# Optimization experiments

Hardware: AMD Instinct MI355X
Metric: run time of the kernel (lower is better)

## Reference

```python
import jax, jax.numpy as jnp
import numpy as np
from functools import partial

B, L, V = 64, 512, 20000
P, M = 150, 6          # total patterns, max pattern length
NEG = -1e9             # semiring zero (log-space)
END_STATES = np.repeat(np.array([3, 4, 5]), 50)  # pattern_len-1 per pattern


@jax.custom_vjp
def ste_heaviside(x):
    return (x > 0).astype(x.dtype)

def _ste_fwd(x):
    return ste_heaviside(x), None

def _ste_bwd(_, g):
    return (g,)  # straight-through identity (matches torch code path)

ste_heaviside.defvjp(_ste_fwd, _ste_bwd)


def setup_inputs() -> dict:
    key = jax.random.key(0)
    ks = jax.random.split(key, 8)
    return {
        "docs": jax.random.randint(ks[0], (B, L), 0, V),
        "doc_lens": jax.random.randint(ks[1], (B,), 1, L),
        "local_embeddings": jax.random.normal(ks[2], (300, V), jnp.float32),
        "diags": jax.random.normal(ks[3], (P * M, 300), jnp.float32) * 0.05,
        "bias": jax.random.normal(ks[4], (P * M, 1), jnp.float32) * 0.05,
        "wildcards": jax.random.normal(ks[5], (P, M - 1), jnp.float32) * 0.05,
        "ln_gamma": jnp.ones((P,), jnp.float32),
        "ln_beta": jnp.zeros((P,), jnp.float32),
        "linear_w": jax.random.normal(ks[6], (2, P), jnp.float32) * 0.05,
        "linear_b": jnp.zeros((2,), jnp.float32),
    }


def reference(docs, doc_lens, local_embeddings, diags, bias, wildcards,
              ln_gamma, ln_beta, linear_w, linear_b):
    end_states = jnp.asarray(END_STATES)                  # [P]
    pat_idx = jnp.arange(P)

    # transition matrices over local vocab, mapped into log-space semiring
    tm_vocab = jax.nn.log_sigmoid((diags @ local_embeddings + bias).T)  # [V, P*M]
    tm = tm_vocab[docs].reshape(B, L, P, M)               # [B,L,P,M]

    # wildcard transitions: semiring.times(one=0, log_sigmoid(wildcards))
    wild = jax.nn.log_sigmoid(wildcards)                  # [P, M-1]

    restart = jnp.zeros((B, P, 1), tm.dtype)              # semiring one
    hid0 = jnp.full((B, P, M), NEG, tm.dtype).at[:, :, 0].set(0.0)
    scores0 = jnp.full((B, P), NEG, tm.dtype)             # semiring zero

    def step(carry, inputs):
        hid, sc = carry
        t, tm_t = inputs                                  # tm_t: [B,P,M]
        main = jnp.concatenate([restart, hid[:, :, :-1] + tm_t[:, :, :-1]], axis=2)
        wildp = jnp.concatenate([restart, hid[:, :, :-1] + wild[None]], axis=2)
        hid = jnp.maximum(main, wildp)                    # semiring plus
        esv = hid[:, pat_idx, end_states]                 # [B,P]
        active = (doc_lens > t)[:, None]
        sc = jnp.where(active, jnp.maximum(sc, esv), sc)
        return (hid, sc), None

    xs = (jnp.arange(L), jnp.moveaxis(tm, 1, 0))          # [L], [L,B,P,M]
    (_, scores), _ = jax.lax.scan(step, (hid0, scores0), xs)

    scores = jnp.exp(scores)                              # from_semiring_to_outer
    mu = scores.mean(axis=-1, keepdims=True)
    var = scores.var(axis=-1, keepdims=True)
    norm = (scores - mu) * jax.lax.rsqrt(var + 1e-5) * ln_gamma + ln_beta
    binar = ste_heaviside(norm)
    return binar @ linear_w.T + linear_b
```

## Files before the change

### kernel.cpp

```cpp
#include <hip/hip_runtime.h>
#include <hip/hip_bf16.h>
#include <hip/hip_fp16.h>
#include <math.h>

#define B_   64
#define L_   512
#define V_   20000
#define P_   150
#define M_   6
#define KDIM 300
#define NOUT 750
#define CWS  752
#define NEGF (-1.0e9f)

#define BM 128
#define BN 128
#define BK 16
#define LDP 132

#define KP 320
#define NIT 10
#define NVG 157
#define NJ  6
#define TILE_U4 1024
#define SA 1024.0f
#define SB 16384.0f
#define INV24 (5.9604644775390625e-8f)

#define TCHUNK 32
#define NCHUNK (L_ / TCHUNK)
#define WARM   5
#define CS_STRIDE 160
#define KVBUF 3

typedef _Float16 f16x8 __attribute__((ext_vector_type(8)));
typedef float f32x16 __attribute__((ext_vector_type(16)));

__device__ __forceinline__ float logsigf(float x) {
    return fminf(x, 0.f) - log1pf(expf(-fabsf(x)));
}

__device__ __forceinline__ float logsigf_fast(float x) {
    return fminf(x, 0.f) - __logf(1.f + __expf(-fabsf(x)));
}

__device__ __forceinline__ void gload_lds16(const void* gp, void* lp) {
    __builtin_amdgcn_global_load_lds(
        (const __attribute__((address_space(1))) unsigned int*)gp,
        (__attribute__((address_space(3))) unsigned int*)lp, 16, 0, 0);
}


__global__ __launch_bounds__(256) void p12_split(
    const float* __restrict__ emb, const float* __restrict__ diags,
    uint4* __restrict__ a_t, uint4* __restrict__ b_t)
{
    __shared__ float T[64][132];
    const int t   = threadIdx.x;
    const int bid = blockIdx.x;

    if (bid < NVG * 5) {
        const int gx = bid % NVG;
        const int ky = bid / NVG;
        const int v0 = gx * 128;
        const int k0 = ky * 64;

        #pragma unroll
        for (int pass = 0; pass < 8; ++pass) {
            int flat = pass * 256 + t;
            int krow = flat >> 5;
            int c4   = (flat & 31) * 4;
            int kg   = k0 + krow;
            int v    = v0 + c4;
            float4 f = {0.f, 0.f, 0.f, 0.f};
            if (kg < KDIM && v + 3 < V_)
                f = *(const float4*)(emb + (size_t)kg * V_ + v);
            *(float4*)&T[krow][c4] = f;
        }
        __syncthreads();

        const int vv = t >> 1;
        const int kh = (t & 1) * 32;
        const int it = ky * 2 + (kh >> 5);
        const int v  = v0 + vv;
        if (v < V_) {
            union { ushort u[8]; uint4 q; } H[4], Lo[4];
            #pragma unroll
            for (int i = 0; i < 32; ++i) {
                float x = T[kh + i][vv] * SA;
                __half h = __float2half_rn(x);
                float rem = x - __half2float(h);
                H[i >> 3].u[i & 7]  = __half_as_ushort(h);
                Lo[i >> 3].u[i & 7] = __half_as_ushort(__float2half_rn(rem));
            }
            uint4* tile = a_t + ((size_t)gx * NIT + it) * TILE_U4;
            #pragma unroll
            for (int c = 0; c < 4; ++c) {
                tile[      c * 128 + vv] = H[c].q;
                tile[512 + c * 128 + vv] = Lo[c].q;
            }
        }
    } else {
        const int bidx = bid - NVG * 5;
        const int it   = bidx % NIT;
        const int j    = bidx / NIT;
        const int row  = t >> 1;
        const int qh   = (t & 1) * 2;
        const int n    = j * 128 + row;
        const bool nok = (n < NOUT);
        const int pm   = nok ? ((n / 5) * 6 + (n % 5)) : 0;
        uint4* tile = b_t + (size_t)bidx * TILE_U4;
        #pragma unroll
        for (int qq = 0; qq < 2; ++qq) {
            int q = qh + qq;
            union { ushort u[8]; uint4 v; } H, Lo;
            #pragma unroll
            for (int e = 0; e < 8; ++e) {
                int k = it * 32 + q * 8 + e;
                float x = (nok && k < KDIM) ? diags[(size_t)pm * KDIM + k] * SB : 0.f;
                __half h = __float2half_rn(x);
                float rem = x - __half2float(h);
                H.u[e]  = __half_as_ushort(h);
                Lo.u[e] = __half_as_ushort(__float2half_rn(rem));
            }
            tile[      q * 128 + row] = H.v;
            tile[512 + q * 128 + row] = Lo.v;
        }
    }
}

__global__ __attribute__((amdgpu_waves_per_eu(2, 2))) __launch_bounds__(256)
void k1m_gemm(
    const uint4* __restrict__ a_t, const uint4* __restrict__ b_t,
    const float* __restrict__ bias, const float* __restrict__ wildc,
    float* __restrict__ cw)
{
    const int bid  = blockIdx.x;
    const int xcd  = bid & 7;
    const int slot = bid >> 3;
    const int g    = xcd + 8 * (slot / 6);
    const int j    = slot % 6;
    if (g >= NVG) return;

    const int t    = threadIdx.x;
    const int lane = t & 63;
    const int w    = t >> 6;
    const int wr   = w >> 1, wc = w & 1;
    const int v0   = g * 128;
    const int n0   = j * 128;

    const int fk16 = lane >> 5;
    const int fm   = lane & 31;

    const uint4* abase = a_t + (size_t)g * NIT * TILE_U4;
    const uint4* bbase = b_t + (size_t)j * NIT * TILE_U4;

    f32x16 acc[2][2];
    #pragma unroll
    for (int i = 0; i < 2; ++i)
        #pragma unroll
        for (int jj = 0; jj < 2; ++jj)
            #pragma unroll
            for (int e = 0; e < 16; ++e) acc[i][jj][e] = 0.f;

    #pragma unroll
    for (int it = 0; it < NIT; ++it) {
        const uint4* atile = abase + (size_t)it * TILE_U4;
        const uint4* btile = bbase + (size_t)it * TILE_U4;
        #pragma unroll
        for (int s = 0; s < 2; ++s) {
            const int q = s * 2 + fk16;
            f16x8 A1[2], A2[2], B1[2], B2[2];
            #pragma unroll
            for (int ri = 0; ri < 2; ++ri) {
                const uint4* ap = atile + q * 128 + wr * 64 + ri * 32 + fm;
                A1[ri] = *(const f16x8*)ap;
                A2[ri] = *(const f16x8*)(ap + 512);
            }
            #pragma unroll
            for (int cj = 0; cj < 2; ++cj) {
                const uint4* bp = btile + q * 128 + wc * 64 + cj * 32 + fm;
                B1[cj] = *(const f16x8*)bp;
                B2[cj] = *(const f16x8*)(bp + 512);
            }
            #pragma unroll
            for (int ri = 0; ri < 2; ++ri)
                #pragma unroll
                for (int cj = 0; cj < 2; ++cj) {
                    acc[ri][cj] = __builtin_amdgcn_mfma_f32_32x32x16_f16(A1[ri], B1[cj], acc[ri][cj], 0, 0, 0);
                    acc[ri][cj] = __builtin_amdgcn_mfma_f32_32x32x16_f16(A1[ri], B2[cj], acc[ri][cj], 0, 0, 0);
                    acc[ri][cj] = __builtin_amdgcn_mfma_f32_32x32x16_f16(A2[ri], B1[cj], acc[ri][cj], 0, 0, 0);
                }
        }
    }

    float biasv[2], lwv[2]; int ncol[2]; bool nok[2];
    #pragma unroll
    for (int cj = 0; cj < 2; ++cj) {
        int n = n0 + wc * 64 + cj * 32 + fm;
        ncol[cj] = n;
        nok[cj]  = (n < NOUT);
        int nc = nok[cj] ? n : 0;
        int pm = (nc / 5) * 6 + (nc % 5);
        biasv[cj] = bias[pm];
        lwv[cj]   = logsigf_fast(wildc[nc]);
    }
    #pragma unroll
    for (int ri = 0; ri < 2; ++ri) {
        int vbase = v0 + wr * 64 + ri * 32 + 4 * fk16;
        #pragma unroll
        for (int cj = 0; cj < 2; ++cj) {
            if (!nok[cj]) continue;
            #pragma unroll
            for (int e = 0; e < 16; ++e) {
                int v = vbase + (e & 3) + 8 * (e >> 2);
                if (v < V_) {
                    float val = acc[ri][cj][e] * INV24 + biasv[cj];
                    cw[(size_t)v * CWS + ncol[cj]] = fmaxf(logsigf_fast(val), lwv[cj]);
                }
            }
        }
    }
}


__global__ __launch_bounds__(256) void k1_gemm_cw(
    const float* __restrict__ emb,
    const float* __restrict__ diags,
    const float* __restrict__ bias,
    const float* __restrict__ wildc,
    float* __restrict__ cw)
{
    __shared__ float As[BK][LDP];
    __shared__ float Bs[BK][LDP];

    const int tid = threadIdx.x;
    const int v0 = blockIdx.x * BM;
    const int n0 = blockIdx.y * BN;
    const int tx = tid & 15;
    const int ty = tid >> 4;

    float acc[8][8];
    #pragma unroll
    for (int i = 0; i < 8; ++i)
        #pragma unroll
        for (int j = 0; j < 8; ++j) acc[i][j] = 0.f;

    const int a_k = tid >> 4;
    const int a_v = (tid & 15) * 8;
    const int b_n   = tid >> 1;
    const int b_kof = (tid & 1) * 8;

    int  brow;
    bool bval;
    {
        int n = n0 + b_n;
        bval = (n < NOUT);
        brow = bval ? ((n / 5) * 6 + (n % 5)) : 0;
    }

    for (int k0 = 0; k0 < KDIM; k0 += BK) {
        {
            float4 f0 = {0,0,0,0}, f1 = {0,0,0,0};
            int k = k0 + a_k;
            if (k < KDIM) {
                const float* src = emb + (size_t)k * V_ + v0 + a_v;
                if (v0 + a_v + 3 < V_) f0 = *(const float4*)src;
                if (v0 + a_v + 7 < V_) f1 = *(const float4*)(src + 4);
            }
            *(float4*)&As[a_k][a_v]     = f0;
            *(float4*)&As[a_k][a_v + 4] = f1;
        }
        {
            float4 f = {0,0,0,0}, g = {0,0,0,0};
            if (bval) {
                const float* src = diags + (size_t)brow * KDIM + k0 + b_kof;
                if (k0 + b_kof + 3 < KDIM) f = *(const float4*)src;
                if (k0 + b_kof + 7 < KDIM) g = *(const float4*)(src + 4);
            }
            Bs[b_kof + 0][b_n] = f.x;
            Bs[b_kof + 1][b_n] = f.y;
            Bs[b_kof + 2][b_n] = f.z;
            Bs[b_kof + 3][b_n] = f.w;
            Bs[b_kof + 4][b_n] = g.x;
            Bs[b_kof + 5][b_n] = g.y;
            Bs[b_kof + 6][b_n] = g.z;
            Bs[b_kof + 7][b_n] = g.w;
        }
        __syncthreads();
        #pragma unroll
        for (int k = 0; k < BK; ++k) {
            float4 a0 = *(const float4*)&As[k][tx * 4];
            float4 a1 = *(const float4*)&As[k][64 + tx * 4];
            float4 b0 = *(const float4*)&Bs[k][ty * 8];
            float4 b1 = *(const float4*)&Bs[k][ty * 8 + 4];
            float av[8] = {a0.x, a0.y, a0.z, a0.w, a1.x, a1.y, a1.z, a1.w};
            float bv[8] = {b0.x, b0.y, b0.z, b0.w, b1.x, b1.y, b1.z, b1.w};
            #pragma unroll
            for (int i = 0; i < 8; ++i)
                #pragma unroll
                for (int j = 0; j < 8; ++j)
                    acc[i][j] = fmaf(av[i], bv[j], acc[i][j]);
        }
        __syncthreads();
    }

    float biasv[8], lwv[8];
    #pragma unroll
    for (int j = 0; j < 8; ++j) {
        int n  = n0 + ty * 8 + j;
        int nc = (n < NOUT) ? n : 0;
        int pm = (nc / 5) * 6 + (nc % 5);
        biasv[j] = bias[pm];
        lwv[j]   = logsigf(wildc[nc]);
    }
    #pragma unroll
    for (int i = 0; i < 8; ++i) {
        int v = v0 + ((i < 4) ? (tx * 4 + i) : (64 + tx * 4 + (i - 4)));
        if (v >= V_) continue;
        float r[8];
        #pragma unroll
        for (int j = 0; j < 8; ++j)
            r[j] = fmaxf(logsigf(acc[i][j] + biasv[j]), lwv[j]);
        float* dst = cw + (size_t)v * CWS + n0 + ty * 8;
        if (n0 + ty * 8     < NOUT) *(float4*)dst       = make_float4(r[0], r[1], r[2], r[3]);
        if (n0 + ty * 8 + 4 < NOUT) *(float4*)(dst + 4) = make_float4(r[4], r[5], r[6], r[7]);
    }
}


__global__ __launch_bounds__(192) void k2_scan(
    const int* __restrict__ docs,
    const int* __restrict__ doc_lens,
    const float* __restrict__ cw,
    float* __restrict__ cs)
{
    const int ci = blockIdx.x;
    const int b  = blockIdx.y;
    const int t0 = ci * TCHUNK;
    const int ts = (t0 >= WARM) ? (t0 - WARM) : 0;
    const int dl = doc_lens[b];
    const int te = min(t0 + TCHUNK, dl);
    const int nt = te - ts;

    __shared__ int   toks[TCHUNK + WARM];
    __shared__ float rows[KVBUF][3][768];

    const int t    = threadIdx.x;
    const int lane = t & 63;
    const int w    = t >> 6;

    if (t < TCHUNK + WARM) {
        int tt = ts + t;
        toks[t] = docs[b * L_ + min(tt, L_ - 1)];
    }
    __syncthreads();

    const int p      = t;
    const int e      = (p < 50) ? 3 : (p < 100) ? 4 : 5;
    const int warm_n = t0 - ts;
    float h1 = NEGF, h2 = NEGF, h3 = NEGF, h4 = NEGF, h5 = NEGF, sc = NEGF;

    const int nrounds = (nt > 0) ? (nt + 2) / 3 : 0;

    for (int r0 = 0; r0 < 2; ++r0) {
        if (r0 >= nrounds) break;
        int idx = min(3 * r0 + w, nt - 1);
        const char* rowp = (const char*)(cw + (size_t)toks[idx] * CWS);
        char* lbase = (char*)&rows[r0][w][0];
        #pragma unroll
        for (int jj = 0; jj < 3; ++jj)
            gload_lds16(rowp + jj * 1024 + lane * 16,
                        lbase + jj * 1024 + lane * 16);
    }

    int bufc = 0;
    for (int r = 0; r < nrounds; ++r) {
        if (r + 1 < nrounds) {
            asm volatile("s_waitcnt vmcnt(3)" ::: "memory");
        } else {
            asm volatile("s_waitcnt vmcnt(0)" ::: "memory");
        }
        __builtin_amdgcn_s_barrier();
        asm volatile("" ::: "memory");

        if (r + 2 < nrounds) {
            int rn  = r + 2;
            int idx = min(3 * rn + w, nt - 1);
            const char* rowp = (const char*)(cw + (size_t)toks[idx] * CWS);
            int bn = bufc + 2; if (bn >= KVBUF) bn -= KVBUF;
            char* lbase = (char*)&rows[bn][w][0];
            #pragma unroll
            for (int jj = 0; jj < 3; ++jj)
                gload_lds16(rowp + jj * 1024 + lane * 16,
                            lbase + jj * 1024 + lane * 16);
        }

        #pragma unroll
        for (int u = 0; u < 3; ++u) {
            int i2 = 3 * r + u;
            if (i2 >= nt) break;
            if (p < P_) {
                const float* rp = &rows[bufc][u][p * 5];
                float c0 = rp[0], c1 = rp[1], c2 = rp[2], c3 = rp[3], c4 = rp[4];
                h5 = h4 + c4;
                h4 = h3 + c3;
                h3 = h2 + c2;
                h2 = h1 + c1;
                h1 = c0;
                if (i2 >= warm_n) {
                    float esv = (e == 3) ? h3 : (e == 4) ? h4 : h5;
                    sc = fmaxf(sc, esv);
                }
            }
        }
        bufc = (bufc + 1 == KVBUF) ? 0 : bufc + 1;
    }
    if (p < P_) cs[(size_t)(b * NCHUNK + ci) * CS_STRIDE + p] = sc;
}

__device__ __forceinline__ float block_sum192(float v, volatile float* red, int tid) {
    #pragma unroll
    for (int off = 32; off > 0; off >>= 1) v += __shfl_down(v, off, 64);
    __syncthreads();
    if ((tid & 63) == 0) red[tid >> 6] = v;
    __syncthreads();
    return red[0] + red[1] + red[2];
}

__global__ __launch_bounds__(192) void k3_final(
    const float* __restrict__ cs,
    const float* __restrict__ gamma,
    const float* __restrict__ beta,
    const float* __restrict__ lw,
    const float* __restrict__ lb,
    float* __restrict__ out)
{
    __shared__ float red[3];
    const int b   = blockIdx.x;
    const int tid = threadIdx.x;
    float s = 0.f;
    if (tid < P_) {
        float m = NEGF;
        const float* row = cs + (size_t)b * NCHUNK * CS_STRIDE + tid;
        #pragma unroll
        for (int ci = 0; ci < NCHUNK; ++ci) m = fmaxf(m, row[ci * CS_STRIDE]);
        s = expf(m);
    }
    float mu = block_sum192(s, red, tid) * (1.f / P_);
    float d  = (tid < P_) ? (s - mu) : 0.f;
    float var = block_sum192(d * d, red, tid) * (1.f / P_);
    float bin = 0.f;
    if (tid < P_) {
        float norm = (s - mu) * rsqrtf(var + 1e-5f) * gamma[tid] + beta[tid];
        bin = (norm > 0.f) ? 1.f : 0.f;
    }
    float o0 = block_sum192((tid < P_) ? bin * lw[tid]      : 0.f, red, tid);
    float o1 = block_sum192((tid < P_) ? bin * lw[P_ + tid] : 0.f, red, tid);
    if (tid == 0) {
        out[b * 2 + 0] = o0 + lb[0];
        out[b * 2 + 1] = o1 + lb[1];
    }
}

extern "C" void kernel_launch(void* const* d_in, const int* in_sizes, int n_in,
                              void* d_out, int out_size, void* d_ws, size_t ws_size,
                              hipStream_t stream)
{
    const int*   docs  = (const int*)  d_in[0];
    const int*   dlens = (const int*)  d_in[1];
    const float* emb   = (const float*)d_in[2];
    const float* diags = (const float*)d_in[3];
    const float* bias  = (const float*)d_in[4];
    const float* wildc = (const float*)d_in[5];
    const float* gamma = (const float*)d_in[6];
    const float* beta  = (const float*)d_in[7];
    const float* lw    = (const float*)d_in[8];
    const float* lb    = (const float*)d_in[9];
    float* out = (float*)d_out;

    const size_t cw_b = (size_t)V_ * CWS * 4;
    const size_t cs_b = (size_t)B_ * NCHUNK * CS_STRIDE * 4;
    const size_t at_b = (size_t)NVG * NIT * TILE_U4 * 16;
    const size_t bt_b = (size_t)NJ  * NIT * TILE_U4 * 16;
    const size_t need = cw_b + cs_b + at_b + bt_b;

    char* base = (char*)d_ws;
    float* cw = (float*)base;
    float* cs = (float*)(base + cw_b);
    uint4* at = (uint4*)(base + cw_b + cs_b);
    uint4* bt = (uint4*)(base + cw_b + cs_b + at_b);

    if (ws_size >= need) {
        p12_split<<<NVG * 5 + NJ * NIT, 256, 0, stream>>>(emb, diags, at, bt);
        k1m_gemm<<<960, 256, 0, stream>>>(at, bt, bias, wildc, cw);
    } else {
        dim3 g1((V_ + BM - 1) / BM, (NOUT + BN - 1) / BN);
        k1_gemm_cw<<<g1, 256, 0, stream>>>(emb, diags, bias, wildc, cw);
    }

    dim3 g2(NCHUNK, B_);
    k2_scan<<<g2, 192, 0, stream>>>(docs, dlens, cw, cs);
    k3_final<<<B_, 192, 0, stream>>>(cs, gamma, beta, lw, lb, out);
}
```

Measured before the change: 154.7 us.

## Replace LDS-staged row prefetch in scan with direct per-thread register prefetch

The scan kernel no longer stages whole vocabulary rows into shared memory with async global-to-LDS loads and barriers. Each thread now loads its own five transition values straight from global memory into registers, keeping two tokens of prefetch in flight. This drops the barriers, the LDS traffic and the shared-memory footprint, but the loads become strided 5-float accesses per thread, which coalesce less well. The GEMM kernel's waves-per-eu hint is also loosened from exactly 2 to at least 4, which may change register allocation.

```diff
diff --git a/kernel.cpp b/kernel.cpp
--- a/kernel.cpp
+++ b/kernel.cpp
@@ -31,7 +31,6 @@
 #define NCHUNK (L_ / TCHUNK)
 #define WARM   5
 #define CS_STRIDE 160
-#define KVBUF 3
 
 typedef _Float16 f16x8 __attribute__((ext_vector_type(8)));
 typedef float f32x16 __attribute__((ext_vector_type(16)));
@@ -42,12 +41,6 @@
 
 __device__ __forceinline__ float logsigf_fast(float x) {
     return fminf(x, 0.f) - __logf(1.f + __expf(-fabsf(x)));
-}
-
-__device__ __forceinline__ void gload_lds16(const void* gp, void* lp) {
-    __builtin_amdgcn_global_load_lds(
-        (const __attribute__((address_space(1))) unsigned int*)gp,
-        (__attribute__((address_space(3))) unsigned int*)lp, 16, 0, 0);
 }
 
 
@@ -129,7 +122,7 @@
     }
 }
 
-__global__ __attribute__((amdgpu_waves_per_eu(2, 2))) __launch_bounds__(256)
+__global__ __attribute__((amdgpu_waves_per_eu(4))) __launch_bounds__(256)
 void k1m_gemm(
     const uint4* __restrict__ a_t, const uint4* __restrict__ b_t,
     const float* __restrict__ bias, const float* __restrict__ wildc,
@@ -343,13 +336,9 @@
     const int te = min(t0 + TCHUNK, dl);
     const int nt = te - ts;
 
-    __shared__ int   toks[TCHUNK + WARM];
-    __shared__ float rows[KVBUF][3][768];
-
-    const int t    = threadIdx.x;
-    const int lane = t & 63;
-    const int w    = t >> 6;
-
+    __shared__ int toks[TCHUNK + WARM];
+
+    const int t = threadIdx.x;
     if (t < TCHUNK + WARM) {
         int tt = ts + t;
         toks[t] = docs[b * L_ + min(tt, L_ - 1)];
@@ -361,60 +350,50 @@
     const int warm_n = t0 - ts;
     float h1 = NEGF, h2 = NEGF, h3 = NEGF, h4 = NEGF, h5 = NEGF, sc = NEGF;
 
-    const int nrounds = (nt > 0) ? (nt + 2) / 3 : 0;
-
-    for (int r0 = 0; r0 < 2; ++r0) {
-        if (r0 >= nrounds) break;
-        int idx = min(3 * r0 + w, nt - 1);
-        const char* rowp = (const char*)(cw + (size_t)toks[idx] * CWS);
-        char* lbase = (char*)&rows[r0][w][0];
-        #pragma unroll
-        for (int jj = 0; jj < 3; ++jj)
-            gload_lds16(rowp + jj * 1024 + lane * 16,
-                        lbase + jj * 1024 + lane * 16);
-    }
-
-    int bufc = 0;
-    for (int r = 0; r < nrounds; ++r) {
-        if (r + 1 < nrounds) {
-            asm volatile("s_waitcnt vmcnt(3)" ::: "memory");
-        } else {
-            asm volatile("s_waitcnt vmcnt(0)" ::: "memory");
-        }
-        __builtin_amdgcn_s_barrier();
-        asm volatile("" ::: "memory");
-
-        if (r + 2 < nrounds) {
-            int rn  = r + 2;
-            int idx = min(3 * rn + w, nt - 1);
-            const char* rowp = (const char*)(cw + (size_t)toks[idx] * CWS);
-            int bn = bufc + 2; if (bn >= KVBUF) bn -= KVBUF;
-            char* lbase = (char*)&rows[bn][w][0];
-            #pragma unroll
-            for (int jj = 0; jj < 3; ++jj)
-                gload_lds16(rowp + jj * 1024 + lane * 16,
-                            lbase + jj * 1024 + lane * 16);
-        }
-
-        #pragma unroll
-        for (int u = 0; u < 3; ++u) {
-            int i2 = 3 * r + u;
-            if (i2 >= nt) break;
-            if (p < P_) {
-                const float* rp = &rows[bufc][u][p * 5];
-                float c0 = rp[0], c1 = rp[1], c2 = rp[2], c3 = rp[3], c4 = rp[4];
-                h5 = h4 + c4;
-                h4 = h3 + c3;
-                h3 = h2 + c2;
-                h2 = h1 + c1;
-                h1 = c0;
-                if (i2 >= warm_n) {
+    if (p < P_ && nt > 0) {
+        const size_t poff = (size_t)p * 5;
+        float A0 = 0, A1 = 0, A2 = 0, A3 = 0, A4 = 0;
+        float B0 = 0, B1 = 0, B2 = 0, B3 = 0, B4 = 0;
+        {
+            const float* r = cw + (size_t)toks[0] * CWS + poff;
+            A0 = r[0]; A1 = r[1]; A2 = r[2]; A3 = r[3]; A4 = r[4];
+        }
+        if (nt > 1) {
+            const float* r = cw + (size_t)toks[1] * CWS + poff;
+            B0 = r[0]; B1 = r[1]; B2 = r[2]; B3 = r[3]; B4 = r[4];
+        }
+        for (int i = 0; i < nt; i += 2) {
+            float c0 = A0, c1 = A1, c2 = A2, c3 = A3, c4 = A4;
+            if (i + 2 < nt) {
+                const float* r = cw + (size_t)toks[i + 2] * CWS + poff;
+                A0 = r[0]; A1 = r[1]; A2 = r[2]; A3 = r[3]; A4 = r[4];
+            }
+            h5 = h4 + c4;
+            h4 = h3 + c3;
+            h3 = h2 + c2;
+            h2 = h1 + c1;
+            h1 = c0;
+            if (i >= warm_n) {
+                float esv = (e == 3) ? h3 : (e == 4) ? h4 : h5;
+                sc = fmaxf(sc, esv);
+            }
+            if (i + 1 < nt) {
+                float d0 = B0, d1 = B1, d2 = B2, d3 = B3, d4 = B4;
+                if (i + 3 < nt) {
+                    const float* r = cw + (size_t)toks[i + 3] * CWS + poff;
+                    B0 = r[0]; B1 = r[1]; B2 = r[2]; B3 = r[3]; B4 = r[4];
+                }
+                h5 = h4 + d4;
+                h4 = h3 + d3;
+                h3 = h2 + d2;
+                h2 = h1 + d1;
+                h1 = d0;
+                if (i + 1 >= warm_n) {
                     float esv = (e == 3) ? h3 : (e == 4) ? h4 : h5;
                     sc = fmaxf(sc, esv);
                 }
             }
         }
-        bufc = (bufc + 1 == KVBUF) ? 0 : bufc + 1;
     }
     if (p < P_) cs[(size_t)(b * NCHUNK + ci) * CS_STRIDE + p] = sc;
 }
```

New measurement: 158.8 us. 2.7% more time.
